# Optimization experiments

Hardware: AMD Instinct MI355X
Metric: run time of the kernel (lower is better)

Reference implementation:

```python
import jax, jax.numpy as jnp
import numpy as np

M_FUZZ = 2.0        # self.m
EPSILON = 1e-8      # self.Epsilon
MAX_ITER = 25       # self.max_iterion


def setup_inputs() -> dict:
    key = jax.random.key(0)
    k1, k2 = jax.random.split(key)
    data = jax.random.normal(k1, (300000, 64), dtype=jnp.float32)
    u0_raw = jax.random.uniform(k2, (300000, 64), dtype=jnp.float32)
    return {"data": data, "u0_raw": u0_raw, "cluster": 64}


def reference(data, u0_raw, cluster):
    # Fuzzy c-means, faithful to GranularComputing.forward:
    #   iterate: C = center(U); U = update(U, C); C_new = center(U);
    #            stop if ||C_new - C||_F < Epsilon; return C (pre-update center).
    m = M_FUZZ
    p = 2.0 / (m - 1.0)  # exponent in membership update (== 2.0)
    N, D = data.shape

    # initialize_matrix_U: random rows normalized to sum to 1
    U0 = u0_raw / jnp.sum(u0_raw, axis=1, keepdims=True)  # [N, c]

    def center(U):
        Um = U ** m                                        # [N, c]
        num = Um.T @ data                                  # [c, D]
        den = jnp.sum(Um, axis=0)[:, None]                 # [c, 1]
        return num / den

    x2 = jnp.sum(data * data, axis=1, keepdims=True)       # [N, 1]

    def sqdist(C):
        # squared Euclidean distances [N, c] via expansion (no N x c x D tensor)
        c2 = jnp.sum(C * C, axis=1)                        # [c]
        return jnp.maximum(x2 + c2 - 2.0 * (data @ C.T), 0.0)

    def step(carry, _):
        U, C_ret, done = carry
        C = center(U)                                      # [c, D]
        # u_ij = 1 / sum_k (d_ij / d_ik)^p  ==  d_ij^{-p} / sum_k d_ik^{-p}
        w = sqdist(C) ** (-p / 2.0)                        # [N, c]
        U_new = w / jnp.sum(w, axis=1, keepdims=True)
        C_new = center(U_new)
        diff = jnp.sqrt(jnp.sum((C_new - C) ** 2))
        # freeze state after convergence (emulates the early break)
        U_out = jnp.where(done, U, U_new)
        C_out = jnp.where(done, C_ret, C)
        return (U_out, C_out, done | (diff < EPSILON)), None

    C0 = jnp.zeros((cluster, D), dtype=data.dtype)
    (_, V, _), _ = jax.lax.scan(
        step, (U0, C0, jnp.array(False)), None, length=MAX_ITER + 1
    )
    return V  # [cluster, D]
```

## Files before the change

### kernel.cpp

```cpp
#include <hip/hip_runtime.h>


#define DM 64
#define CL 64
#define PARTIAL_STRIDE 4160
#define MAX_ITER 25
#define MAX_BLOCKS 1024
#define LDP 72

typedef __attribute__((ext_vector_type(8))) short bf16x8;
typedef __attribute__((ext_vector_type(4))) float f32x4;

__device__ __forceinline__ unsigned f2bf1(float f) {
  unsigned u = __builtin_bit_cast(unsigned, f);
  return (u + 0x7FFFu + ((u >> 16) & 1u)) >> 16;
}
__device__ __forceinline__ unsigned pkbf(float a, float b) {
  return f2bf1(a) | (f2bf1(b) << 16);
}

__device__ __forceinline__ float wave_sum(float v) {
#define DPPADD(ctrl, rmask)                                                  \
  v += __builtin_bit_cast(float, __builtin_amdgcn_update_dpp(                \
           0, __builtin_bit_cast(int, v), ctrl, rmask, 0xf, false));
  DPPADD(0x111, 0xf)
  DPPADD(0x112, 0xf)
  DPPADD(0x114, 0xf)
  DPPADD(0x118, 0xf)
  DPPADD(0x142, 0xa)
  DPPADD(0x143, 0xc)
#undef DPPADD
  return __builtin_bit_cast(
      float, __builtin_amdgcn_readlane(__builtin_bit_cast(int, v), 63));
}

__device__ __forceinline__ float group16_sum(float v) {
#define DPPADD(ctrl)                                                         \
  v += __builtin_bit_cast(float, __builtin_amdgcn_update_dpp(                \
           0, __builtin_bit_cast(int, v), ctrl, 0xf, 0xf, false));
  DPPADD(0xB1)
  DPPADD(0x4E)
  DPPADD(0x141)
  DPPADD(0x140)
#undef DPPADD
  return v;
}

__global__ void fcm_prep(const float* __restrict__ data, float* __restrict__ x2,
                         float* __restrict__ diffac, int* __restrict__ done,
                         int* __restrict__ ticket, int N) {
  int i = blockIdx.x * blockDim.x + threadIdx.x;
  if (i == 0) { *diffac = 0.0f; *done = 0; *ticket = 0; }
  if (i < N) {
    const float4* r = (const float4*)(data + (size_t)i * DM);
    float s = 0.0f;
#pragma unroll
    for (int q = 0; q < DM / 4; q++) {
      float4 v = r[q];
      s = fmaf(v.x, v.x, s); s = fmaf(v.y, v.y, s);
      s = fmaf(v.z, v.z, s); s = fmaf(v.w, v.w, s);
    }
    x2[i] = s;
  }
}

template <bool INIT>
__global__ __launch_bounds__(256, 3)
void fcm_pass(const float* __restrict__ data, const float* __restrict__ x2,
              const float* __restrict__ CU,
              float* __restrict__ partial, const int* __restrict__ done,
              int N, int ntiles) {
  if (!INIT && *done) return;
  __shared__ __align__(16) unsigned short Xb[64 * LDP];
  __shared__ __align__(16) unsigned short XTb[64 * LDP];
  __shared__ __align__(16) unsigned short umT[64 * LDP];
  __shared__ __align__(16) float rpart[4 * 64];
  __shared__ __align__(16) float rrs[64];
  __shared__ __align__(16) float x2s[64];

  const int tid  = threadIdx.x;
  const int w    = __builtin_amdgcn_readfirstlane(tid >> 6);
  const int col  = tid & 15;
  const int quad = (tid >> 4) & 3;

  bf16x8 cf0, cf1;
  float c2j = 0.0f;
  if (!INIT) {
    const float* crow = CU + (size_t)(16 * w + col) * DM;
    float4 ca = *(const float4*)(crow + quad * 8);
    float4 cb = *(const float4*)(crow + quad * 8 + 4);
    float4 cc = *(const float4*)(crow + 32 + quad * 8);
    float4 cd = *(const float4*)(crow + 32 + quad * 8 + 4);
    float cp = ca.x*ca.x + ca.y*ca.y + ca.z*ca.z + ca.w*ca.w
             + cb.x*cb.x + cb.y*cb.y + cb.z*cb.z + cb.w*cb.w
             + cc.x*cc.x + cc.y*cc.y + cc.z*cc.z + cc.w*cc.w
             + cd.x*cd.x + cd.y*cd.y + cd.z*cd.z + cd.w*cd.w;
    cp += __shfl_xor(cp, 16, 64);
    cp += __shfl_xor(cp, 32, 64);
    c2j = cp;
    union { bf16x8 v; unsigned u[4]; } P0, P1;
    P0.u[0] = pkbf(ca.x, ca.y); P0.u[1] = pkbf(ca.z, ca.w);
    P0.u[2] = pkbf(cb.x, cb.y); P0.u[3] = pkbf(cb.z, cb.w);
    P1.u[0] = pkbf(cc.x, cc.y); P1.u[1] = pkbf(cc.z, cc.w);
    P1.u[2] = pkbf(cd.x, cd.y); P1.u[3] = pkbf(cd.z, cd.w);
    cf0 = P0.v; cf1 = P1.v;
  }

  f32x4 D2[4];
#pragma unroll
  for (int dt = 0; dt < 4; dt++) D2[dt] = f32x4{0.f, 0.f, 0.f, 0.f};
  float den = 0.0f;

  for (int t = blockIdx.x; t < ntiles; t += gridDim.x) {
    const int base = t * 64;
    const int np = min(64, N - base);
    __syncthreads();

    for (int i = tid; i < 1024; i += 256) {
      int p = i >> 4;
      int d4 = (i & 15) * 4;
      float4 v = {0.f, 0.f, 0.f, 0.f};
      if (p < np) v = *(const float4*)(data + (size_t)(base + p) * DM + d4);
      unsigned long long w64 = (unsigned long long)pkbf(v.x, v.y) |
                               ((unsigned long long)pkbf(v.z, v.w) << 32);
      *(unsigned long long*)(void*)&Xb[p * LDP + d4] = w64;
      XTb[(d4 + 0) * LDP + p] = (unsigned short)f2bf1(v.x);
      XTb[(d4 + 1) * LDP + p] = (unsigned short)f2bf1(v.y);
      XTb[(d4 + 2) * LDP + p] = (unsigned short)f2bf1(v.z);
      XTb[(d4 + 3) * LDP + p] = (unsigned short)f2bf1(v.w);
    }
    if (tid < 64) x2s[tid] = (base + tid < N) ? x2[base + tid] : 0.0f;
    __syncthreads();

    float W[4][4];
    if (INIT) {
#pragma unroll
      for (int pt = 0; pt < 4; pt++)
#pragma unroll
        for (int r = 0; r < 4; r++) {
          int pl = pt * 16 + quad * 4 + r;
          W[pt][r] = (pl < np)
              ? CU[(size_t)(base + pl) * CL + 16 * w + col] : 0.0f;
        }
    } else {
#pragma unroll
      for (int pt = 0; pt < 4; pt++) {
        bf16x8 a0 = *(const bf16x8*)(const void*)&Xb[(pt * 16 + col) * LDP + quad * 8];
        bf16x8 a1 = *(const bf16x8*)(const void*)&Xb[(pt * 16 + col) * LDP + 32 + quad * 8];
        f32x4 s = f32x4{0.f, 0.f, 0.f, 0.f};
        s = __builtin_amdgcn_mfma_f32_16x16x32_bf16(a0, cf0, s, 0, 0, 0);
        s = __builtin_amdgcn_mfma_f32_16x16x32_bf16(a1, cf1, s, 0, 0, 0);
        f32x4 x2v = *(const f32x4*)(const void*)&x2s[pt * 16 + quad * 4];
#pragma unroll
        for (int r = 0; r < 4; r++) {
          float dist = fmaxf(fmaf(-2.0f, s[r], x2v[r] + c2j), 0.0f);
          W[pt][r] = __builtin_amdgcn_rcpf(dist);
        }
      }
    }

    float rs[4][4];
#pragma unroll
    for (int pt = 0; pt < 4; pt++)
#pragma unroll
      for (int r = 0; r < 4; r++) rs[pt][r] = group16_sum(W[pt][r]);
    if (col == 0) {
#pragma unroll
      for (int pt = 0; pt < 4; pt++) {
        float4 v4 = {rs[pt][0], rs[pt][1], rs[pt][2], rs[pt][3]};
        *(float4*)(void*)&rpart[w * 64 + pt * 16 + quad * 4] = v4;
      }
    }
    __syncthreads();
    if (tid < 64) {
      float rt = rpart[tid] + rpart[64 + tid] + rpart[128 + tid] + rpart[192 + tid];
      rrs[tid] = __builtin_amdgcn_rcpf(rt);
    }
    __syncthreads();

#pragma unroll
    for (int pt = 0; pt < 4; pt++) {
      f32x4 rrv = *(const f32x4*)(const void*)&rrs[pt * 16 + quad * 4];
      float um[4];
#pragma unroll
      for (int r = 0; r < 4; r++) {
        float u = W[pt][r] * rrv[r];
        float m = u * u;
        um[r] = (pt * 16 + quad * 4 + r < np) ? m : 0.0f;
        den += um[r];
      }
      unsigned long long w64 = (unsigned long long)pkbf(um[0], um[1]) |
                               ((unsigned long long)pkbf(um[2], um[3]) << 32);
      *(unsigned long long*)(void*)&umT[(16 * w + col) * LDP + pt * 16 + quad * 4] = w64;
    }

#pragma unroll
    for (int pb = 0; pb < 2; pb++) {
      bf16x8 au = *(const bf16x8*)(const void*)&umT[(16 * w + col) * LDP + pb * 32 + quad * 8];
#pragma unroll
      for (int dt = 0; dt < 4; dt++) {
        bf16x8 bx = *(const bf16x8*)(const void*)&XTb[(dt * 16 + col) * LDP + pb * 32 + quad * 8];
        D2[dt] = __builtin_amdgcn_mfma_f32_16x16x32_bf16(au, bx, D2[dt], 0, 0, 0);
      }
    }
  }

  den += __shfl_xor(den, 16, 64);
  den += __shfl_xor(den, 32, 64);
  float* pb = partial + (size_t)blockIdx.x * PARTIAL_STRIDE;
  if (quad == 0) pb[CL * DM + 16 * w + col] = den;
#pragma unroll
  for (int dt = 0; dt < 4; dt++)
#pragma unroll
    for (int r = 0; r < 4; r++)
      pb[(size_t)(16 * w + quad * 4 + r) * DM + dt * 16 + col] = D2[dt][r];
}

__global__ __launch_bounds__(1024, 1)
void fcm_reduce(const float* __restrict__ partial, float* __restrict__ Cnew,
                const float* __restrict__ Cold, float* __restrict__ out,
                float* __restrict__ diffac, int* __restrict__ done,
                int* __restrict__ ticket, int compute_diff, int nb) {
  if (compute_diff && *done) return;
  __shared__ float sm[16 * 64];
  __shared__ float sden[1024];
  __shared__ int lastflag;
  __shared__ float sdiff;
  int j = blockIdx.x;
  int tid = threadIdx.x;
  int d = tid & 63;
  int slice = tid >> 6;
  float s = 0.0f;
  for (int b = slice; b < nb; b += 16)
    s += partial[(size_t)b * PARTIAL_STRIDE + j * DM + d];
  sm[slice * 64 + d] = s;
  float dv = 0.0f;
  for (int b = tid; b < nb; b += 1024)
    dv += partial[(size_t)b * PARTIAL_STRIDE + CL * DM + j];
  sden[tid] = dv;
  __syncthreads();
#pragma unroll
  for (int st = 8; st; st >>= 1) {
    if (slice < st) sm[slice * 64 + d] += sm[(slice + st) * 64 + d];
    __syncthreads();
  }
#pragma unroll
  for (int st = 512; st >= 64; st >>= 1) {
    if (tid < st) sden[tid] += sden[tid + st];
    __syncthreads();
  }
  if (tid < 64) {
    float denj = wave_sum(sden[tid]);
    float c = sm[tid] / denj;
    Cnew[j * DM + tid] = c;
    if (compute_diff) {
      float df = c - Cold[j * DM + tid];
      float tot = wave_sum(df * df);
      if (tid == 0) atomicAdd(diffac, tot);
    }
  }
  if (!compute_diff) return;
  __syncthreads();
  if (tid == 0) {
    __threadfence();
    int t = atomicAdd(ticket, 1);
    lastflag = (t == (int)gridDim.x - 1);
  }
  __syncthreads();
  if (!lastflag) return;
  if (tid == 0) sdiff = atomicAdd(diffac, 0.0f);
  __syncthreads();
  if (sdiff < 1e-16f) {
    for (int i = tid; i < CL * DM; i += 1024) out[i] = Cold[i];
    if (tid == 0) *done = 1;
  }
  if (tid == 0) { *diffac = 0.0f; *ticket = 0; }
}

__global__ void fcm_final(const float* __restrict__ Clast, float* __restrict__ out,
                          const int* __restrict__ done) {
  if (*done) return;
  int i = blockIdx.x * blockDim.x + threadIdx.x;
  if (i < CL * DM) out[i] = Clast[i];
}

extern "C" void kernel_launch(void* const* d_in, const int* in_sizes, int n_in,
                              void* d_out, int out_size, void* d_ws, size_t ws_size,
                              hipStream_t stream) {
  const float* data = (const float*)d_in[0];
  const float* u0   = (const float*)d_in[1];
  float* out = (float*)d_out;
  int N = in_sizes[0] / DM;
  int ntiles = (N + 63) / 64;

  float* ws = (float*)d_ws;
  size_t Noff = ((size_t)N + 15) & ~(size_t)15;
  float* x2 = ws;
  float* C0 = ws + Noff;
  float* C1 = C0 + CL * DM;
  float* diffac = C1 + CL * DM;
  int* done = (int*)(diffac + 1);
  int* ticket = (int*)(diffac + 2);
  float* partial = diffac + 16;

  size_t used = Noff + 2 * CL * DM + 16;
  size_t avail = (ws_size / 4 > used) ? (ws_size / 4 - used) / PARTIAL_STRIDE : 0;
  int nb = (int)(avail < MAX_BLOCKS ? avail : MAX_BLOCKS);
  if (nb < 1) nb = 1;

  hipLaunchKernelGGL(fcm_prep, dim3((N + 255) / 256), dim3(256), 0, stream,
                     data, x2, diffac, done, ticket, N);
  hipLaunchKernelGGL((fcm_pass<true>), dim3(nb), dim3(256), 0, stream,
                     data, x2, u0, partial, done, N, ntiles);
  hipLaunchKernelGGL(fcm_reduce, dim3(64), dim3(1024), 0, stream,
                     partial, C0, C1, out, diffac, done, ticket, 0, nb);

  float* bufs[2] = {C0, C1};
  for (int k = 0; k < MAX_ITER; k++) {
    float* Cc = bufs[k & 1];
    float* Cn = bufs[(k + 1) & 1];
    hipLaunchKernelGGL((fcm_pass<false>), dim3(nb), dim3(256), 0, stream,
                       data, x2, Cc, partial, done, N, ntiles);
    hipLaunchKernelGGL(fcm_reduce, dim3(64), dim3(1024), 0, stream,
                       partial, Cn, Cc, out, diffac, done, ticket, 1, nb);
  }
  hipLaunchKernelGGL(fcm_final, dim3(16), dim3(256), 0, stream,
                     bufs[1], out, done);
}
```

Before: 432.4 us.

## Pre-convert data to bf16 once and stream half-size rows each iteration

The prep kernel now writes a bf16 copy of the data matrix into workspace. Every pass kernel loads 16-byte bf16 vectors instead of converting fp32 rows per tile, which halves global traffic per iteration and drops the per-element conversion work. The maximum block count is also lowered from 1024 to 512, which means fewer partial sums to reduce. The costs are one extra bf16 write of the full dataset and more workspace used.

Result: no change. 427.1 us (-1.2%).

```diff
diff --git a/kernel.cpp b/kernel.cpp
--- a/kernel.cpp
+++ b/kernel.cpp
@@ -5,7 +5,7 @@
 #define CL 64
 #define PARTIAL_STRIDE 4160
 #define MAX_ITER 25
-#define MAX_BLOCKS 1024
+#define MAX_BLOCKS 512
 #define LDP 72
 
 typedef __attribute__((ext_vector_type(8))) short bf16x8;
@@ -47,18 +47,22 @@
 }
 
 __global__ void fcm_prep(const float* __restrict__ data, float* __restrict__ x2,
+                         unsigned short* __restrict__ xbf,
                          float* __restrict__ diffac, int* __restrict__ done,
                          int* __restrict__ ticket, int N) {
   int i = blockIdx.x * blockDim.x + threadIdx.x;
   if (i == 0) { *diffac = 0.0f; *done = 0; *ticket = 0; }
   if (i < N) {
     const float4* r = (const float4*)(data + (size_t)i * DM);
+    unsigned short* xo = xbf + (size_t)i * DM;
     float s = 0.0f;
 #pragma unroll
     for (int q = 0; q < DM / 4; q++) {
       float4 v = r[q];
       s = fmaf(v.x, v.x, s); s = fmaf(v.y, v.y, s);
       s = fmaf(v.z, v.z, s); s = fmaf(v.w, v.w, s);
+      uint2 pk = {pkbf(v.x, v.y), pkbf(v.z, v.w)};
+      *(uint2*)(void*)(xo + q * 4) = pk;
     }
     x2[i] = s;
   }
@@ -66,7 +70,7 @@
 
 template <bool INIT>
 __global__ __launch_bounds__(256, 3)
-void fcm_pass(const float* __restrict__ data, const float* __restrict__ x2,
+void fcm_pass(const unsigned short* __restrict__ xbf, const float* __restrict__ x2,
               const float* __restrict__ CU,
               float* __restrict__ partial, const int* __restrict__ done,
               int N, int ntiles) {
@@ -116,18 +120,15 @@
     const int np = min(64, N - base);
     __syncthreads();
 
-    for (int i = tid; i < 1024; i += 256) {
-      int p = i >> 4;
-      int d4 = (i & 15) * 4;
-      float4 v = {0.f, 0.f, 0.f, 0.f};
-      if (p < np) v = *(const float4*)(data + (size_t)(base + p) * DM + d4);
-      unsigned long long w64 = (unsigned long long)pkbf(v.x, v.y) |
-                               ((unsigned long long)pkbf(v.z, v.w) << 32);
-      *(unsigned long long*)(void*)&Xb[p * LDP + d4] = w64;
-      XTb[(d4 + 0) * LDP + p] = (unsigned short)f2bf1(v.x);
-      XTb[(d4 + 1) * LDP + p] = (unsigned short)f2bf1(v.y);
-      XTb[(d4 + 2) * LDP + p] = (unsigned short)f2bf1(v.z);
-      XTb[(d4 + 3) * LDP + p] = (unsigned short)f2bf1(v.w);
+    for (int i = tid; i < 512; i += 256) {
+      int p = i >> 3;
+      int d8 = (i & 7) * 8;
+      bf16x8 v = bf16x8{0, 0, 0, 0, 0, 0, 0, 0};
+      if (p < np) v = *(const bf16x8*)(xbf + (size_t)(base + p) * DM + d8);
+      *(bf16x8*)(void*)&Xb[p * LDP + d8] = v;
+#pragma unroll
+      for (int k = 0; k < 8; k++)
+        XTb[(d8 + k) * LDP + p] = (unsigned short)v[k];
     }
     if (tid < 64) x2s[tid] = (base + tid < N) ? x2[base + tid] : 0.0f;
     __syncthreads();
@@ -296,22 +297,23 @@
   float* ws = (float*)d_ws;
   size_t Noff = ((size_t)N + 15) & ~(size_t)15;
   float* x2 = ws;
-  float* C0 = ws + Noff;
+  unsigned short* xbf = (unsigned short*)(ws + Noff);
+  float* C0 = ws + Noff + (size_t)N * 32;
   float* C1 = C0 + CL * DM;
   float* diffac = C1 + CL * DM;
   int* done = (int*)(diffac + 1);
   int* ticket = (int*)(diffac + 2);
   float* partial = diffac + 16;
 
-  size_t used = Noff + 2 * CL * DM + 16;
+  size_t used = Noff + (size_t)N * 32 + 2 * CL * DM + 16;
   size_t avail = (ws_size / 4 > used) ? (ws_size / 4 - used) / PARTIAL_STRIDE : 0;
   int nb = (int)(avail < MAX_BLOCKS ? avail : MAX_BLOCKS);
   if (nb < 1) nb = 1;
 
   hipLaunchKernelGGL(fcm_prep, dim3((N + 255) / 256), dim3(256), 0, stream,
-                     data, x2, diffac, done, ticket, N);
+                     data, x2, xbf, diffac, done, ticket, N);
   hipLaunchKernelGGL((fcm_pass<true>), dim3(nb), dim3(256), 0, stream,
-                     data, x2, u0, partial, done, N, ntiles);
+                     xbf, x2, u0, partial, done, N, ntiles);
   hipLaunchKernelGGL(fcm_reduce, dim3(64), dim3(1024), 0, stream,
                      partial, C0, C1, out, diffac, done, ticket, 0, nb);
 
@@ -320,7 +322,7 @@
     float* Cc = bufs[k & 1];
     float* Cn = bufs[(k + 1) & 1];
     hipLaunchKernelGGL((fcm_pass<false>), dim3(nb), dim3(256), 0, stream,
-                       data, x2, Cc, partial, done, N, ntiles);
+                       xbf, x2, Cc, partial, done, N, ntiles);
     hipLaunchKernelGGL(fcm_reduce, dim3(64), dim3(1024), 0, stream,
                        partial, Cn, Cc, out, diffac, done, ticket, 1, nb);
   }
```
